# Kernel tuning notes

Hardware: AMD Instinct MI355X
Metric: run time of the kernel (lower is better)

## Reference

```python
import jax, jax.numpy as jnp
import numpy as np

B, T, H, U = 4, 512, 512, 256

def setup_inputs() -> dict:
    key = jax.random.key(0)
    k1, k2, k3, k4 = jax.random.split(key, 4)
    h = jax.random.normal(k1, (B, T, H), dtype=jnp.float32)
    s_q = (6.0 / (H + U)) ** 0.5  # glorot_uniform limits
    W_q = jax.random.uniform(k2, (H, U), minval=-s_q, maxval=s_q, dtype=jnp.float32)
    W_k = jax.random.uniform(k3, (H, U), minval=-s_q, maxval=s_q, dtype=jnp.float32)
    b_q = jnp.zeros((U,), dtype=jnp.float32)
    s_w = (6.0 / (U + 1)) ** 0.5
    W = jax.random.uniform(k4, (U, 1), minval=-s_w, maxval=s_w, dtype=jnp.float32)
    b_alpha = jnp.zeros((1,), dtype=jnp.float32)
    return {"h": h, "W_q": W_q, "W_k": W_k, "b_q": b_q, "W": W, "b_alpha": b_alpha}

def reference(h, W_q, W_k, b_q, W, b_alpha):
    # h: (B, T, H)
    h_q = jnp.einsum('bth,hu->btu', h, W_q)          # (B, T, U)
    h_k = jnp.einsum('bth,hu->btu', h, W_k)          # (B, T, U)
    # pairwise additive score: q[b,t,t',u] = tanh(h_q[b,t,u] + h_k[b,t',u] + b_q[u])
    q = jnp.tanh(h_q[:, :, None, :] + h_k[:, None, :, :] + b_q)  # (B, T, T, U)
    score = jax.nn.sigmoid(jnp.einsum('btsu,uo->bts', q, W) + b_alpha[0])  # (B, T, T)
    alpha = jax.nn.softmax(score, axis=-1)           # softmax over t'
    context_per_t = jnp.einsum('bts,bsh->bth', alpha, h)  # (B, T, H)
    context = jnp.mean(context_per_t, axis=1)        # (B, H)
    return context
```

## Files before the change

kernel.cpp:

```cpp
#include <hip/hip_runtime.h>

#define BB 4
#define TT 512
#define HH 512
#define UU 256

#define C2L2E 2.8853900817779268f
#define L2E   1.4426950408889634f

typedef __attribute__((ext_vector_type(8))) short bf16x8;
typedef __attribute__((ext_vector_type(4))) float f32x4;
typedef __attribute__((ext_vector_type(2))) float f32x2;

static __device__ inline unsigned short f2bf(float x) {
    union { float f; unsigned u; } v; v.f = x;
    unsigned r = v.u + 0x7fff + ((v.u >> 16) & 1);
    return (unsigned short)(r >> 16);
}

static __device__ inline f32x2 pk_mul(f32x2 a, f32x2 b) {
    f32x2 d; asm("v_pk_mul_f32 %0, %1, %2" : "=v"(d) : "v"(a), "v"(b)); return d;
}
static __device__ inline f32x2 pk_add(f32x2 a, f32x2 b) {
    f32x2 d; asm("v_pk_add_f32 %0, %1, %2" : "=v"(d) : "v"(a), "v"(b)); return d;
}
static __device__ inline f32x2 pk_fma(f32x2 a, f32x2 b, f32x2 c) {
    f32x2 d; asm("v_pk_fma_f32 %0, %1, %2, %3" : "=v"(d) : "v"(a), "v"(b), "v"(c)); return d;
}

__global__ __launch_bounds__(256) void prep_kernel(const float* __restrict__ h,
                                                   const float* __restrict__ Wq,
                                                   const float* __restrict__ Wk,
                                                   const float* __restrict__ bq,
                                                   const float* __restrict__ W,
                                                   const float* __restrict__ b_alpha,
                                                   unsigned short* __restrict__ hbf,
                                                   unsigned short* __restrict__ WcatT,
                                                   float* __restrict__ cbq,
                                                   float* __restrict__ w2,
                                                   float* __restrict__ w2p,
                                                   float* __restrict__ scal,
                                                   float* __restrict__ denom,
                                                   float* __restrict__ wsum,
                                                   float* __restrict__ out)
{
    const int blk = blockIdx.x;
    const int tid = threadIdx.x;

    if (blk < 256) {
        const int gid = blk * 256 + tid;
#pragma unroll
        for (int it = 0; it < 4; ++it) {
            const int i = gid + it * 65536;
            const float4 v = ((const float4*)h)[i];
            ushort4 o;
            o.x = f2bf(v.x); o.y = f2bf(v.y); o.z = f2bf(v.z); o.w = f2bf(v.w);
            ((ushort4*)hbf)[i] = o;
        }
    } else if (blk < 512) {
        __shared__ unsigned short lds[32][33];
        const int tile = blk - 256;
        const int tn = tile & 15;
        const int tk = tile >> 4;
        const int lx = tid & 31;
        const int ly = tid >> 5;
        const int n = tn * 32 + lx;
#pragma unroll
        for (int kk = ly; kk < 32; kk += 8) {
            const int k = tk * 32 + kk;
            const float v = (n < 256) ? Wq[k * UU + n] : Wk[k * UU + (n - 256)];
            lds[lx][kk] = f2bf(C2L2E * v);
        }
        __syncthreads();
#pragma unroll
        for (int nn = ly; nn < 32; nn += 8) {
            WcatT[(size_t)(tn * 32 + nn) * 512 + tk * 32 + lx] = lds[nn][lx];
        }
    } else {
        __shared__ float red[256];
        const float w = W[tid];
        w2[tid] = -2.0f * w;
        red[tid] = w;
        cbq[tid] = C2L2E * bq[tid];
        if (tid < 64) {
            w2p[2 * tid]     = -2.0f * (W[4 * tid]     + W[4 * tid + 2]);
            w2p[2 * tid + 1] = -2.0f * (W[4 * tid + 1] + W[4 * tid + 3]);
        }
        __syncthreads();
        for (int off = 128; off > 0; off >>= 1) {
            if (tid < off) red[tid] += red[tid + off];
            __syncthreads();
        }
        if (tid == 0) { scal[0] = red[0]; scal[1] = b_alpha[0]; }
#pragma unroll
        for (int it = 0; it < 8; ++it) {
            const int i = tid + it * 256;
            denom[i] = 0.0f; wsum[i] = 0.0f; out[i] = 0.0f;
        }
    }
}

__global__ __launch_bounds__(256) void qk_mfma(const unsigned short* __restrict__ hbf,
                                               const unsigned short* __restrict__ WcatT,
                                               const float* __restrict__ cbq,
                                               float* __restrict__ EQ,
                                               float* __restrict__ EKm)
{
    const int wave = (blockIdx.x * 256 + threadIdx.x) >> 6;
    const int lane = threadIdx.x & 63;
    const int mt = wave >> 4;
    const int nt = wave & 15;
    const int m0 = mt * 16, n0 = nt * 32;
    const int lrow = lane & 15;
    const int kgrp = lane >> 4;

    f32x4 acc0 = {0.f, 0.f, 0.f, 0.f};
    f32x4 acc1 = {0.f, 0.f, 0.f, 0.f};
    const unsigned short* Arow = hbf   + (size_t)(m0 + lrow) * 512 + kgrp * 8;
    const unsigned short* B0   = WcatT + (size_t)(n0 + lrow) * 512 + kgrp * 8;
    const unsigned short* B1   = B0 + (size_t)16 * 512;

#pragma unroll
    for (int k0 = 0; k0 < 512; k0 += 32) {
        const bf16x8 a  = *(const bf16x8*)(Arow + k0);
        const bf16x8 b0 = *(const bf16x8*)(B0 + k0);
        const bf16x8 b1 = *(const bf16x8*)(B1 + k0);
        acc0 = __builtin_amdgcn_mfma_f32_16x16x32_bf16(a, b0, acc0, 0, 0, 0);
        acc1 = __builtin_amdgcn_mfma_f32_16x16x32_bf16(a, b1, acc1, 0, 0, 0);
    }

    const int n_0 = n0 + lrow;
    const int n_1 = n_0 + 16;
    if (nt < 8) {
#pragma unroll
        for (int r = 0; r < 4; r++) {
            const int m = m0 + kgrp * 4 + r;
            EQ[(size_t)(n_0 >> 2) * 8192 + m * 4 + (n_0 & 3)] = __builtin_amdgcn_exp2f(acc0[r]);
            EQ[(size_t)(n_1 >> 2) * 8192 + m * 4 + (n_1 & 3)] = __builtin_amdgcn_exp2f(acc1[r]);
        }
    } else {
        const float bias0 = cbq[n_0 - 256];
        const float bias1 = cbq[n_1 - 256];
#pragma unroll
        for (int r = 0; r < 4; r++) {
            const int m = m0 + kgrp * 4 + r;
            EKm[(size_t)m * 256 + (n_0 - 256)] = __builtin_amdgcn_exp2f(acc0[r] + bias0);
            EKm[(size_t)m * 256 + (n_1 - 256)] = __builtin_amdgcn_exp2f(acc1[r] + bias1);
        }
    }
}

__global__ __launch_bounds__(256, 8) void score_kernel(const float* __restrict__ EQ,
                                                       const float* __restrict__ EKm,
                                                       const float* __restrict__ w2,
                                                       const float* __restrict__ w2p,
                                                       const float* __restrict__ scal,
                                                       float* __restrict__ E,
                                                       float* __restrict__ denom)
{
    const int b  = blockIdx.z;
    const int tg = blockIdx.y;
    const int sg = blockIdx.x;
    const int tid  = threadIdx.x;
    const int lane = tid & 63;
    const int wv = __builtin_amdgcn_readfirstlane((int)(tid >> 6));
    const int g  = b * TT + tg * 64 + lane;

    __shared__ float khk[2048];
    __shared__ float w2l[256];
    __shared__ float w2pl[128];
    __shared__ float red[4][64];

    {
        const float* srcb = EKm + (size_t)(b * TT + sg * 8) * 256;
        *(float4*)&khk[tid * 4]        = *(const float4*)(srcb + tid * 4);
        *(float4*)&khk[tid * 4 + 1024] = *(const float4*)(srcb + tid * 4 + 1024);
        w2l[tid] = w2[tid];
        if (tid < 128) w2pl[tid] = w2p[tid];
    }
    __syncthreads();

    const float sumW    = scal[0];
    const float b_alpha = scal[1];
    const f32x2 kOne = {1.0f, 1.0f};

    const float* __restrict__ ek0b = &khk[(2 * wv + 0) * 256];
    const float* __restrict__ ek1b = &khk[(2 * wv + 1) * 256];

    float acc[2][2] = {{0.f, 0.f}, {0.f, 0.f}};

    for (int uc = 0; uc < UU; uc += 16) {
        f32x4 hr[4];
#pragma unroll
        for (int q = 0; q < 4; q++)
            hr[q] = *(const f32x4*)(EQ + (size_t)(uc / 4 + q) * 8192 + g * 4);
#pragma unroll
        for (int qd = 0; qd < 4; ++qd) {
            const int u = uc + 4 * qd;
            const f32x2 hf01 = __builtin_shufflevector(hr[qd], hr[qd], 0, 1);
            const f32x2 hf23 = __builtin_shufflevector(hr[qd], hr[qd], 2, 3);
            const f32x4 wv4  = *(const f32x4*)&w2l[u];
            const f32x2 w01  = __builtin_shufflevector(wv4, wv4, 0, 1);
            const f32x2 w23  = __builtin_shufflevector(wv4, wv4, 2, 3);
            const f32x2 wp   = *(const f32x2*)&w2pl[u >> 1];
#pragma unroll
            for (int si = 0; si < 2; ++si) {
                const float* __restrict__ ekb = si ? ek1b : ek0b;
                const f32x4 ekv  = *(const f32x4*)&ekb[u];
                const f32x2 ek01 = __builtin_shufflevector(ekv, ekv, 0, 1);
                const f32x2 ek23 = __builtin_shufflevector(ekv, ekv, 2, 3);
                const f32x2 ev0 = pk_mul(hf01, ek01);
                const f32x2 ev1 = pk_mul(hf23, ek23);
                const f32x2 t   = pk_add(ev0, kOne);
                const f32x2 d   = pk_fma(t, ev1, t);
                f32x2 n = pk_fma(w01, ev1, wp);
                n = pk_fma(w23, ev0, n);
                const float dq = d.x * d.y;
                const float nq = fmaf(n.y, d.x, n.x * d.y);
                const float r  = __builtin_amdgcn_rcpf(dq);
                acc[si][qd & 1] = fmaf(nq, r, acc[si][qd & 1]);
            }
        }
    }

    const int s0 = sg * 8 + wv * 2;
    float Ev[2];
    float part = 0.0f;
#pragma unroll
    for (int si = 0; si < 2; ++si) {
        const float z   = acc[si][0] + acc[si][1] + sumW + b_alpha;
        const float sgm = __builtin_amdgcn_rcpf(1.0f + __builtin_amdgcn_exp2f(-z * L2E));
        const float e   = __builtin_amdgcn_exp2f(sgm * L2E);
        Ev[si] = e;
        part += e;
    }

    float* __restrict__ Erow = E + (size_t)g * TT + s0;
    *(float2*)Erow = make_float2(Ev[0], Ev[1]);

    red[wv][lane] = part;
    __syncthreads();
    if (wv == 0) {
        const float tot = red[0][lane] + red[1][lane] + red[2][lane] + red[3][lane];
        atomicAdd(&denom[g], tot);
    }
}

__global__ __launch_bounds__(256) void colsum_kernel(const float* __restrict__ E,
                                                     const float* __restrict__ denom,
                                                     float* __restrict__ wsum)
{
    const int b  = blockIdx.y;
    const int t0 = blockIdx.x * 4;
    const int s  = threadIdx.x;
    float a0 = 0.0f, a1 = 0.0f;
#pragma unroll
    for (int ti = 0; ti < 4; ++ti) {
        const int t = t0 + ti;
        const float rd = 1.0f / denom[b * TT + t];
        const float* __restrict__ Er = E + (size_t)(b * TT + t) * TT;
        a0 = fmaf(Er[s],       rd, a0);
        a1 = fmaf(Er[s + 256], rd, a1);
    }
    atomicAdd(&wsum[b * TT + s],       a0 * (1.0f / TT));
    atomicAdd(&wsum[b * TT + s + 256], a1 * (1.0f / TT));
}

__global__ __launch_bounds__(512) void ctx_kernel(const float* __restrict__ h,
                                                  const float* __restrict__ wsum,
                                                  float* __restrict__ out)
{
    const int b  = blockIdx.y;
    const int s0 = blockIdx.x * 8;
    const int hd = threadIdx.x;
    float a = 0.0f;
#pragma unroll
    for (int si = 0; si < 8; ++si) {
        const int s = s0 + si;
        a = fmaf(wsum[b * TT + s], h[(size_t)(b * TT + s) * HH + hd], a);
    }
    atomicAdd(&out[b * HH + hd], a);
}

extern "C" void kernel_launch(void* const* d_in, const int* in_sizes, int n_in,
                              void* d_out, int out_size, void* d_ws, size_t ws_size,
                              hipStream_t stream)
{
    const float* h       = (const float*)d_in[0];
    const float* Wq      = (const float*)d_in[1];
    const float* Wk      = (const float*)d_in[2];
    const float* bq      = (const float*)d_in[3];
    const float* W       = (const float*)d_in[4];
    const float* b_alpha = (const float*)d_in[5];
    float* out = (float*)d_out;

    float* ws    = (float*)d_ws;
    float* EQ    = ws;
    float* EKm   = EQ + (size_t)524288;
    float* E     = EKm + (size_t)524288;
    float* denom = E + (size_t)1048576;
    float* wsum  = denom + BB * TT;
    float* w2    = wsum + BB * TT;
    float* w2p   = w2 + UU;
    float* scal  = w2p + 128;
    float* cbq   = scal + 2;

    unsigned short* hbf   = (unsigned short*)E;
    unsigned short* WcatT = hbf + (size_t)1048576;

    prep_kernel  <<<513, 256, 0, stream>>>(h, Wq, Wk, bq, W, b_alpha,
                                           hbf, WcatT, cbq, w2, w2p, scal, denom, wsum, out);
    qk_mfma      <<<512, 256, 0, stream>>>(hbf, WcatT, cbq, EQ, EKm);
    score_kernel <<<dim3(64, 8, BB), 256, 0, stream>>>(EQ, EKm, w2, w2p, scal, E, denom);
    colsum_kernel<<<dim3(128, BB), 256, 0, stream>>>(E, denom, wsum);
    ctx_kernel   <<<dim3(64, BB), 512, 0, stream>>>(h, wsum, out);
}
```

Before: 74.70 us.

## Restructure score kernel: split U across waves, two t rows per lane, prescaled K

The score kernel now uses 512-thread blocks that each cover 128 query rows. Each wave handles a 32-wide slice of the U dimension for all 8 key columns, and each lane computes two query rows so every LDS K value is reused twice. K is premultiplied by a permuted w2 in shared memory, which removes two packed FMAs per inner step. The partial sums are reduced across waves through a larger shared buffer, and the denominator is combined with LDS atomics before the global atomic. The trade-offs are more LDS, more live registers (16 accumulators under a 512-thread launch bound) and a second barrier for the cross-wave reduction.

Measured after the change: 67.24 us. 1.11x faster.

```diff
diff --git a/kernel.cpp b/kernel.cpp
--- a/kernel.cpp
+++ b/kernel.cpp
@@ -150,7 +150,7 @@
     }
 }
 
-__global__ __launch_bounds__(256, 8) void score_kernel(const float* __restrict__ EQ,
+__global__ __launch_bounds__(512, 8) void score_kernel(const float* __restrict__ EQ,
                                                        const float* __restrict__ EKm,
                                                        const float* __restrict__ w2,
                                                        const float* __restrict__ w2p,
@@ -164,86 +164,119 @@
     const int tid  = threadIdx.x;
     const int lane = tid & 63;
     const int wv = __builtin_amdgcn_readfirstlane((int)(tid >> 6));
-    const int g  = b * TT + tg * 64 + lane;
-
-    __shared__ float khk[2048];
-    __shared__ float w2l[256];
-    __shared__ float w2pl[128];
-    __shared__ float red[4][64];
+    const int gA = b * TT + tg * 128 + lane;
+    const int gB = gA + 64;
+
+    __shared__ __align__(16) float khk [8 * 256];
+    __shared__ __align__(16) float khkp[8 * 256];
+    __shared__ __align__(16) float part[8 * 2 * 8 * 64];
+    __shared__ float dnm[128];
 
     {
-        const float* srcb = EKm + (size_t)(b * TT + sg * 8) * 256;
-        *(float4*)&khk[tid * 4]        = *(const float4*)(srcb + tid * 4);
-        *(float4*)&khk[tid * 4 + 1024] = *(const float4*)(srcb + tid * 4 + 1024);
-        w2l[tid] = w2[tid];
-        if (tid < 128) w2pl[tid] = w2p[tid];
+        const int flat = tid * 4;
+        const int s = flat >> 8;
+        const int u = flat & 255;
+        const float4 ek4 = *(const float4*)(EKm + (size_t)(b * TT + sg * 8 + s) * 256 + u);
+        const float4 w4  = *(const float4*)(w2 + u);
+        *(float4*)&khk[flat] = ek4;
+        float4 ep;
+        ep.x = ek4.x * w4.z; ep.y = ek4.y * w4.w;
+        ep.z = ek4.z * w4.x; ep.w = ek4.w * w4.y;
+        *(float4*)&khkp[flat] = ep;
+        if (tid < 128) dnm[tid] = 0.0f;
+    }
+    __syncthreads();
+
+    const float* __restrict__ wpw = w2p + wv * 16;
+
+    float accA[8], accB[8];
+#pragma unroll
+    for (int s = 0; s < 8; ++s) { accA[s] = 0.0f; accB[s] = 0.0f; }
+
+    const int uq0 = wv * 8;
+
+    for (int sub = 0; sub < 4; ++sub) {
+        const int q0 = uq0 + sub * 2;
+        const f32x4 hA0 = *(const f32x4*)(EQ + (size_t)(q0    ) * 8192 + gA * 4);
+        const f32x4 hA1 = *(const f32x4*)(EQ + (size_t)(q0 + 1) * 8192 + gA * 4);
+        const f32x4 hB0 = *(const f32x4*)(EQ + (size_t)(q0    ) * 8192 + gB * 4);
+        const f32x4 hB1 = *(const f32x4*)(EQ + (size_t)(q0 + 1) * 8192 + gB * 4);
+#pragma unroll
+        for (int s = 0; s < 8; ++s) {
+#pragma unroll
+            for (int q = 0; q < 2; ++q) {
+                const int uu = (q0 + q) * 4;
+                const f32x4 ekv  = *(const f32x4*)&khk [s * 256 + uu];
+                const f32x4 ekpv = *(const f32x4*)&khkp[s * 256 + uu];
+                const f32x2 ek01  = __builtin_shufflevector(ekv,  ekv,  0, 1);
+                const f32x2 ek23  = __builtin_shufflevector(ekv,  ekv,  2, 3);
+                const f32x2 ekp01 = __builtin_shufflevector(ekpv, ekpv, 0, 1);
+                const f32x2 ekp23 = __builtin_shufflevector(ekpv, ekpv, 2, 3);
+                const f32x2 wp2 = { wpw[(sub * 2 + q) * 2], wpw[(sub * 2 + q) * 2 + 1] };
+                const f32x4 hA = q ? hA1 : hA0;
+                const f32x4 hB = q ? hB1 : hB0;
+                const f32x2 hA01 = __builtin_shufflevector(hA, hA, 0, 1);
+                const f32x2 hA23 = __builtin_shufflevector(hA, hA, 2, 3);
+                const f32x2 hB01 = __builtin_shufflevector(hB, hB, 0, 1);
+                const f32x2 hB23 = __builtin_shufflevector(hB, hB, 2, 3);
+                {
+                    const f32x2 ev0 = pk_mul(hA01, ek01);
+                    const f32x2 ev1 = pk_mul(hA23, ek23);
+                    const f32x2 t   = pk_add(ev0, (f32x2){1.0f, 1.0f});
+                    const f32x2 d   = pk_fma(t, ev1, t);
+                    f32x2 n = pk_fma(hA01, ekp01, wp2);
+                    n = pk_fma(hA23, ekp23, n);
+                    const float dq = d.x * d.y;
+                    const float nq = fmaf(n.y, d.x, n.x * d.y);
+                    const float r  = __builtin_amdgcn_rcpf(dq);
+                    accA[s] = fmaf(nq, r, accA[s]);
+                }
+                {
+                    const f32x2 ev0 = pk_mul(hB01, ek01);
+                    const f32x2 ev1 = pk_mul(hB23, ek23);
+                    const f32x2 t   = pk_add(ev0, (f32x2){1.0f, 1.0f});
+                    const f32x2 d   = pk_fma(t, ev1, t);
+                    f32x2 n = pk_fma(hB01, ekp01, wp2);
+                    n = pk_fma(hB23, ekp23, n);
+                    const float dq = d.x * d.y;
+                    const float nq = fmaf(n.y, d.x, n.x * d.y);
+                    const float r  = __builtin_amdgcn_rcpf(dq);
+                    accB[s] = fmaf(nq, r, accB[s]);
+                }
+            }
+        }
+    }
+
+#pragma unroll
+    for (int s = 0; s < 8; ++s) {
+        part[((s * 2 + 0) * 8 + wv) * 64 + lane] = accA[s];
+        part[((s * 2 + 1) * 8 + wv) * 64 + lane] = accB[s];
     }
     __syncthreads();
 
     const float sumW    = scal[0];
     const float b_alpha = scal[1];
-    const f32x2 kOne = {1.0f, 1.0f};
-
-    const float* __restrict__ ek0b = &khk[(2 * wv + 0) * 256];
-    const float* __restrict__ ek1b = &khk[(2 * wv + 1) * 256];
-
-    float acc[2][2] = {{0.f, 0.f}, {0.f, 0.f}};
-
-    for (int uc = 0; uc < UU; uc += 16) {
-        f32x4 hr[4];
-#pragma unroll
-        for (int q = 0; q < 4; q++)
-            hr[q] = *(const f32x4*)(EQ + (size_t)(uc / 4 + q) * 8192 + g * 4);
-#pragma unroll
-        for (int qd = 0; qd < 4; ++qd) {
-            const int u = uc + 4 * qd;
-            const f32x2 hf01 = __builtin_shufflevector(hr[qd], hr[qd], 0, 1);
-            const f32x2 hf23 = __builtin_shufflevector(hr[qd], hr[qd], 2, 3);
-            const f32x4 wv4  = *(const f32x4*)&w2l[u];
-            const f32x2 w01  = __builtin_shufflevector(wv4, wv4, 0, 1);
-            const f32x2 w23  = __builtin_shufflevector(wv4, wv4, 2, 3);
-            const f32x2 wp   = *(const f32x2*)&w2pl[u >> 1];
-#pragma unroll
-            for (int si = 0; si < 2; ++si) {
-                const float* __restrict__ ekb = si ? ek1b : ek0b;
-                const f32x4 ekv  = *(const f32x4*)&ekb[u];
-                const f32x2 ek01 = __builtin_shufflevector(ekv, ekv, 0, 1);
-                const f32x2 ek23 = __builtin_shufflevector(ekv, ekv, 2, 3);
-                const f32x2 ev0 = pk_mul(hf01, ek01);
-                const f32x2 ev1 = pk_mul(hf23, ek23);
-                const f32x2 t   = pk_add(ev0, kOne);
-                const f32x2 d   = pk_fma(t, ev1, t);
-                f32x2 n = pk_fma(w01, ev1, wp);
-                n = pk_fma(w23, ev0, n);
-                const float dq = d.x * d.y;
-                const float nq = fmaf(n.y, d.x, n.x * d.y);
-                const float r  = __builtin_amdgcn_rcpf(dq);
-                acc[si][qd & 1] = fmaf(nq, r, acc[si][qd & 1]);
-            }
-        }
-    }
-
-    const int s0 = sg * 8 + wv * 2;
+    const int t_local = tid & 127;
+    const int sh = tid >> 7;
+    const int st = t_local >> 6;
+    const int li = t_local & 63;
     float Ev[2];
-    float part = 0.0f;
-#pragma unroll
-    for (int si = 0; si < 2; ++si) {
-        const float z   = acc[si][0] + acc[si][1] + sumW + b_alpha;
+#pragma unroll
+    for (int k = 0; k < 2; ++k) {
+        const int s = sh * 2 + k;
+        const float* pp = &part[(s * 2 + st) * 8 * 64 + li];
+        float z = 0.0f;
+#pragma unroll
+        for (int w = 0; w < 8; ++w) z += pp[w * 64];
+        z += sumW + b_alpha;
         const float sgm = __builtin_amdgcn_rcpf(1.0f + __builtin_amdgcn_exp2f(-z * L2E));
-        const float e   = __builtin_amdgcn_exp2f(sgm * L2E);
-        Ev[si] = e;
-        part += e;
-    }
-
-    float* __restrict__ Erow = E + (size_t)g * TT + s0;
-    *(float2*)Erow = make_float2(Ev[0], Ev[1]);
-
-    red[wv][lane] = part;
+        Ev[k] = __builtin_amdgcn_exp2f(sgm * L2E);
+    }
+    const int grow = b * TT + tg * 128 + t_local;
+    *(float2*)(E + (size_t)grow * TT + sg * 8 + sh * 2) = make_float2(Ev[0], Ev[1]);
+    atomicAdd(&dnm[t_local], Ev[0] + Ev[1]);
     __syncthreads();
-    if (wv == 0) {
-        const float tot = red[0][lane] + red[1][lane] + red[2][lane] + red[3][lane];
-        atomicAdd(&denom[g], tot);
-    }
+    if (tid < 128) atomicAdd(&denom[b * TT + tg * 128 + tid], dnm[tid]);
 }
 
 __global__ __launch_bounds__(256) void colsum_kernel(const float* __restrict__ E,
@@ -311,7 +344,7 @@
     prep_kernel  <<<513, 256, 0, stream>>>(h, Wq, Wk, bq, W, b_alpha,
                                            hbf, WcatT, cbq, w2, w2p, scal, denom, wsum, out);
     qk_mfma      <<<512, 256, 0, stream>>>(hbf, WcatT, cbq, EQ, EKm);
-    score_kernel <<<dim3(64, 8, BB), 256, 0, stream>>>(EQ, EKm, w2, w2p, scal, E, denom);
+    score_kernel <<<dim3(64, 4, BB), 512, 0, stream>>>(EQ, EKm, w2, w2p, scal, E, denom);
     colsum_kernel<<<dim3(128, BB), 256, 0, stream>>>(E, denom, wsum);
     ctx_kernel   <<<dim3(64, BB), 512, 0, stream>>>(h, wsum, out);
 }
```

## Retile score kernel: split U across waves, 4x4 register tile per thread

Applied to the files above, without the earlier changes.

The score kernel is retiled so each block covers 256 query rows and 4 key columns. Each wave now handles a 64-wide slice of the U dimension, and every thread accumulates a 4x4 (key x query) register tile, so each loaded EQ or EK value feeds several score terms. Partial sums across waves are reduced through shared memory, then each thread writes a float4 of E and issues one atomic per row. The larger tile increases register pressure, so launch bounds drop from 8 to 4 blocks per CU, and the extra LDS reduction adds a synchronization step.

Measured after the change: 68.36 us. 8.5% less time.

```diff
diff --git a/kernel.cpp b/kernel.cpp
--- a/kernel.cpp
+++ b/kernel.cpp
@@ -150,7 +150,7 @@
     }
 }
 
-__global__ __launch_bounds__(256, 8) void score_kernel(const float* __restrict__ EQ,
+__global__ __launch_bounds__(256, 4) void score_kernel(const float* __restrict__ EQ,
                                                        const float* __restrict__ EKm,
                                                        const float* __restrict__ w2,
                                                        const float* __restrict__ w2p,
@@ -164,86 +164,93 @@
     const int tid  = threadIdx.x;
     const int lane = tid & 63;
     const int wv = __builtin_amdgcn_readfirstlane((int)(tid >> 6));
-    const int g  = b * TT + tg * 64 + lane;
-
-    __shared__ float khk[2048];
-    __shared__ float w2l[256];
-    __shared__ float w2pl[128];
-    __shared__ float red[4][64];
+    const int gbase = b * TT + tg * 256;
+    const int g0 = gbase + lane;
+
+    __shared__ __align__(16) float khk [4 * 256];
+    __shared__ __align__(16) float part[4 * 4 * 4 * 64];
 
     {
-        const float* srcb = EKm + (size_t)(b * TT + sg * 8) * 256;
-        *(float4*)&khk[tid * 4]        = *(const float4*)(srcb + tid * 4);
-        *(float4*)&khk[tid * 4 + 1024] = *(const float4*)(srcb + tid * 4 + 1024);
-        w2l[tid] = w2[tid];
-        if (tid < 128) w2pl[tid] = w2p[tid];
-    }
+        const int flat = tid * 4;
+        const int s = flat >> 8;
+        const int u = flat & 255;
+        *(float4*)&khk[flat] = *(const float4*)(EKm + (size_t)(b * TT + sg * 4 + s) * 256 + u);
+    }
+    __syncthreads();
+
+    float acc[4][4];
+#pragma unroll
+    for (int s = 0; s < 4; ++s)
+#pragma unroll
+        for (int st = 0; st < 4; ++st) acc[s][st] = 0.0f;
+
+    const int q00 = wv * 16;
+
+    for (int sub = 0; sub < 8; ++sub) {
+        const int q0 = q00 + sub * 2;
+        f32x4 hq[4][2];
+#pragma unroll
+        for (int st = 0; st < 4; ++st) {
+#pragma unroll
+            for (int q = 0; q < 2; ++q)
+                hq[st][q] = *(const f32x4*)(EQ + (size_t)(q0 + q) * 8192 + (g0 + st * 64) * 4);
+        }
+        f32x2 w01[2], w23[2], wp[2];
+#pragma unroll
+        for (int q = 0; q < 2; ++q) {
+            w01[q] = *(const f32x2*)(w2 + (q0 + q) * 4);
+            w23[q] = *(const f32x2*)(w2 + (q0 + q) * 4 + 2);
+            wp[q]  = *(const f32x2*)(w2p + (q0 + q) * 2);
+        }
+#pragma unroll
+        for (int s = 0; s < 4; ++s) {
+#pragma unroll
+            for (int q = 0; q < 2; ++q) {
+                const f32x4 ekv  = *(const f32x4*)&khk[s * 256 + (q0 + q) * 4];
+                const f32x2 ek01 = __builtin_shufflevector(ekv, ekv, 0, 1);
+                const f32x2 ek23 = __builtin_shufflevector(ekv, ekv, 2, 3);
+#pragma unroll
+                for (int st = 0; st < 4; ++st) {
+                    const f32x2 h01 = __builtin_shufflevector(hq[st][q], hq[st][q], 0, 1);
+                    const f32x2 h23 = __builtin_shufflevector(hq[st][q], hq[st][q], 2, 3);
+                    const f32x2 ev0 = pk_mul(h01, ek01);
+                    const f32x2 ev1 = pk_mul(h23, ek23);
+                    const f32x2 t   = pk_add(ev0, (f32x2){1.0f, 1.0f});
+                    const f32x2 d   = pk_fma(t, ev1, t);
+                    f32x2 n = pk_fma(w01[q], ev1, wp[q]);
+                    n = pk_fma(w23[q], ev0, n);
+                    const float dq = d.x * d.y;
+                    const float nq = fmaf(n.y, d.x, n.x * d.y);
+                    const float r  = __builtin_amdgcn_rcpf(dq);
+                    acc[s][st] = fmaf(nq, r, acc[s][st]);
+                }
+            }
+        }
+    }
+
+#pragma unroll
+    for (int s = 0; s < 4; ++s)
+#pragma unroll
+        for (int st = 0; st < 4; ++st)
+            part[((s * 4 + st) * 4 + wv) * 64 + lane] = acc[s][st];
     __syncthreads();
 
     const float sumW    = scal[0];
     const float b_alpha = scal[1];
-    const f32x2 kOne = {1.0f, 1.0f};
-
-    const float* __restrict__ ek0b = &khk[(2 * wv + 0) * 256];
-    const float* __restrict__ ek1b = &khk[(2 * wv + 1) * 256];
-
-    float acc[2][2] = {{0.f, 0.f}, {0.f, 0.f}};
-
-    for (int uc = 0; uc < UU; uc += 16) {
-        f32x4 hr[4];
-#pragma unroll
-        for (int q = 0; q < 4; q++)
-            hr[q] = *(const f32x4*)(EQ + (size_t)(uc / 4 + q) * 8192 + g * 4);
-#pragma unroll
-        for (int qd = 0; qd < 4; ++qd) {
-            const int u = uc + 4 * qd;
-            const f32x2 hf01 = __builtin_shufflevector(hr[qd], hr[qd], 0, 1);
-            const f32x2 hf23 = __builtin_shufflevector(hr[qd], hr[qd], 2, 3);
-            const f32x4 wv4  = *(const f32x4*)&w2l[u];
-            const f32x2 w01  = __builtin_shufflevector(wv4, wv4, 0, 1);
-            const f32x2 w23  = __builtin_shufflevector(wv4, wv4, 2, 3);
-            const f32x2 wp   = *(const f32x2*)&w2pl[u >> 1];
-#pragma unroll
-            for (int si = 0; si < 2; ++si) {
-                const float* __restrict__ ekb = si ? ek1b : ek0b;
-                const f32x4 ekv  = *(const f32x4*)&ekb[u];
-                const f32x2 ek01 = __builtin_shufflevector(ekv, ekv, 0, 1);
-                const f32x2 ek23 = __builtin_shufflevector(ekv, ekv, 2, 3);
-                const f32x2 ev0 = pk_mul(hf01, ek01);
-                const f32x2 ev1 = pk_mul(hf23, ek23);
-                const f32x2 t   = pk_add(ev0, kOne);
-                const f32x2 d   = pk_fma(t, ev1, t);
-                f32x2 n = pk_fma(w01, ev1, wp);
-                n = pk_fma(w23, ev0, n);
-                const float dq = d.x * d.y;
-                const float nq = fmaf(n.y, d.x, n.x * d.y);
-                const float r  = __builtin_amdgcn_rcpf(dq);
-                acc[si][qd & 1] = fmaf(nq, r, acc[si][qd & 1]);
-            }
-        }
-    }
-
-    const int s0 = sg * 8 + wv * 2;
-    float Ev[2];
-    float part = 0.0f;
-#pragma unroll
-    for (int si = 0; si < 2; ++si) {
-        const float z   = acc[si][0] + acc[si][1] + sumW + b_alpha;
+    const int est = tid >> 6;
+    float Ev[4];
+    float psum = 0.0f;
+#pragma unroll
+    for (int s = 0; s < 4; ++s) {
+        const float* pp = &part[(s * 4 + est) * 4 * 64 + lane];
+        float z = pp[0] + pp[64] + pp[128] + pp[192] + sumW + b_alpha;
         const float sgm = __builtin_amdgcn_rcpf(1.0f + __builtin_amdgcn_exp2f(-z * L2E));
-        const float e   = __builtin_amdgcn_exp2f(sgm * L2E);
-        Ev[si] = e;
-        part += e;
-    }
-
-    float* __restrict__ Erow = E + (size_t)g * TT + s0;
-    *(float2*)Erow = make_float2(Ev[0], Ev[1]);
-
-    red[wv][lane] = part;
-    __syncthreads();
-    if (wv == 0) {
-        const float tot = red[0][lane] + red[1][lane] + red[2][lane] + red[3][lane];
-        atomicAdd(&denom[g], tot);
-    }
+        Ev[s] = __builtin_amdgcn_exp2f(sgm * L2E);
+        psum += Ev[s];
+    }
+    const int grow = gbase + tid;
+    *(float4*)(E + (size_t)grow * TT + sg * 4) = make_float4(Ev[0], Ev[1], Ev[2], Ev[3]);
+    atomicAdd(&denom[grow], psum);
 }
 
 __global__ __launch_bounds__(256) void colsum_kernel(const float* __restrict__ E,
@@ -311,7 +318,7 @@
     prep_kernel  <<<513, 256, 0, stream>>>(h, Wq, Wk, bq, W, b_alpha,
                                            hbf, WcatT, cbq, w2, w2p, scal, denom, wsum, out);
     qk_mfma      <<<512, 256, 0, stream>>>(hbf, WcatT, cbq, EQ, EKm);
-    score_kernel <<<dim3(64, 8, BB), 256, 0, stream>>>(EQ, EKm, w2, w2p, scal, E, denom);
+    score_kernel <<<dim3(128, 2, BB), 256, 0, stream>>>(EQ, EKm, w2, w2p, scal, E, denom);
     colsum_kernel<<<dim3(128, BB), 256, 0, stream>>>(E, denom, wsum);
     ctx_kernel   <<<dim3(64, BB), 512, 0, stream>>>(h, wsum, out);
 }
```
